# Performance work log

Measured on AMD Instinct MI355X. Metric: run time of the kernel, lower is better.

## Reference

```python
import jax, jax.numpy as jnp
import numpy as np

B, N, E, H = 2, 2048, 1024, 16
D = E // H


def setup_inputs() -> dict:
    key = jax.random.key(0)
    ks = jax.random.split(key, 10)
    s = 0.02  # small init so softmax is well-conditioned
    return {
        "x": jax.random.normal(ks[0], (B, N, E), jnp.float32),
        "y": jax.random.normal(ks[1], (B, N, E), jnp.float32),
        # W stored as [in, out]; torch Linear computes x @ W_t.T + b, equivalent here.
        "Wq": jax.random.normal(ks[2], (E, E), jnp.float32) * s,
        "bq": jax.random.normal(ks[3], (E,), jnp.float32) * s,
        "Wk": jax.random.normal(ks[4], (E, E), jnp.float32) * s,
        "bk": jax.random.normal(ks[5], (E,), jnp.float32) * s,
        "Wv": jax.random.normal(ks[6], (E, E), jnp.float32) * s,
        "bv": jax.random.normal(ks[7], (E,), jnp.float32) * s,
        "Wo": jax.random.normal(ks[8], (E, E), jnp.float32) * s,
        "bo": jax.random.normal(ks[9], (E,), jnp.float32) * s,
    }


def _split_heads(t):
    # [b, n, (h d)] -> [b, h, n, d]
    b, n, e = t.shape
    return t.reshape(b, n, H, D).transpose(0, 2, 1, 3)


def reference(x, y, Wq, bq, Wk, bk, Wv, bv, Wo, bo):
    q = _split_heads(x @ Wq + bq)          # [b,h,n,d]
    k = _split_heads(y @ Wk + bk)
    v = _split_heads(y @ Wv + bv)
    energy = jnp.einsum('bhqd,bhkd->bhqk', q, k)            # [b,h,n,n]
    # Faithful quirk: softmax first, then divide by sqrt(emb_size).
    scaling = jnp.asarray(E, x.dtype) ** 0.5
    att = jax.nn.softmax(energy, axis=-1) / scaling
    out = jnp.einsum('bhqk,bhkd->bhqd', att, v)             # [b,h,n,d]
    out = out.transpose(0, 2, 1, 3).reshape(x.shape[0], x.shape[1], E)
    return out @ Wo + bo
```

## Files before the change

### kernel.cpp

```cpp
#include <hip/hip_runtime.h>
#include <stdint.h>

#define BATCH 2
#define SEQ   2048
#define EMB   1024
#define NH    16
#define HD    64
#define MROWS (BATCH*SEQ)
#define LOG2E 1.4426950408889634f

using bf16x8 = __attribute__((ext_vector_type(8))) short;
using f32x4  = __attribute__((ext_vector_type(4))) float;
using f32x16 = __attribute__((ext_vector_type(16))) float;

__device__ __forceinline__ unsigned short f2bf(float f) {
  __bf16 b = (__bf16)f;
  return __builtin_bit_cast(unsigned short, b);
}

__device__ __forceinline__ unsigned int cvtpk_bf16(float lo, float hi) {
  unsigned int w;
  asm("v_cvt_pk_bf16_f32 %0, %1, %2" : "=v"(w) : "v"(lo), "v"(hi));
  return w;
}

#if __has_builtin(__builtin_amdgcn_exp2f)
__device__ __forceinline__ float fast_exp2(float x) { return __builtin_amdgcn_exp2f(x); }
#else
__device__ __forceinline__ float fast_exp2(float x) {
  float r;
  asm("v_exp_f32 %0, %1\n\ts_nop 1" : "=v"(r) : "v"(x));
  return r;
}
#endif

__device__ __forceinline__ void swap32(unsigned int& a, unsigned int& b, int hi) {
#if __has_builtin(__builtin_amdgcn_permlane32_swap)
  (void)hi;
  typedef unsigned int u32x2_t __attribute__((ext_vector_type(2)));
  u32x2_t r = __builtin_amdgcn_permlane32_swap(a, b, false, false);
  a = r[0]; b = r[1];
#else
  const unsigned int ca = __shfl_xor(a, 32), cb = __shfl_xor(b, 32);
  const unsigned int na = hi ? cb : a;
  const unsigned int nb = hi ? b : ca;
  a = na; b = nb;
#endif
}

__device__ __forceinline__ float xmax32(float x, int hi) {
  unsigned int a = __builtin_bit_cast(unsigned int, x), b = a;
  swap32(a, b, hi);
  return fmaxf(__builtin_bit_cast(float, a), __builtin_bit_cast(float, b));
}

__device__ __forceinline__ float xadd32(float x, int hi) {
  unsigned int a = __builtin_bit_cast(unsigned int, x), b = a;
  swap32(a, b, hi);
  return __builtin_bit_cast(float, a) + __builtin_bit_cast(float, b);
}

__device__ __forceinline__ void async_load16(const void* g, void* l) {
  __builtin_amdgcn_global_load_lds(
      (__attribute__((address_space(1))) void*)g,
      (__attribute__((address_space(3))) void*)l,
      16, 0, 0);
}

__global__ __launch_bounds__(256) void convert_kernel(
    const float* __restrict__ in, unsigned short* __restrict__ out, int n4) {
  int i = blockIdx.x * blockDim.x + threadIdx.x;
  if (i >= n4) return;
  const float4 v = reinterpret_cast<const float4*>(in)[i];
  ushort4 o;
  o.x = f2bf(v.x); o.y = f2bf(v.y); o.z = f2bf(v.z); o.w = f2bf(v.w);
  reinterpret_cast<ushort4*>(out)[i] = o;
}

__global__ __launch_bounds__(256) void transw_kernel(
    const float* __restrict__ Wq, const float* __restrict__ Wk,
    const float* __restrict__ Wv, const float* __restrict__ Wo,
    unsigned short* __restrict__ WtAll) {
  const int z = blockIdx.z;
  const float* W = (z == 0) ? Wq : (z == 1) ? Wk : (z == 2) ? Wv : Wo;
  unsigned short* Wt = WtAll + (size_t)z * EMB * EMB;
  __shared__ unsigned short tile[64][65];
  const int tc = threadIdx.x & 15;
  const int tr = threadIdx.x >> 4;
  const int n0 = blockIdx.x * 64, k0 = blockIdx.y * 64;
#pragma unroll
  for (int rr = 0; rr < 4; ++rr) {
    const int row = rr * 16 + tr;
    float4 v = *reinterpret_cast<const float4*>(W + (size_t)(k0 + row) * EMB + n0 + tc * 4);
    tile[tc * 4 + 0][row] = f2bf(v.x);
    tile[tc * 4 + 1][row] = f2bf(v.y);
    tile[tc * 4 + 2][row] = f2bf(v.z);
    tile[tc * 4 + 3][row] = f2bf(v.w);
  }
  __syncthreads();
#pragma unroll
  for (int rr = 0; rr < 4; ++rr) {
    const int row = rr * 16 + tr;
    ushort4 o;
    o.x = tile[row][tc * 4 + 0];
    o.y = tile[row][tc * 4 + 1];
    o.z = tile[row][tc * 4 + 2];
    o.w = tile[row][tc * 4 + 3];
    *reinterpret_cast<ushort4*>(Wt + (size_t)(n0 + row) * EMB + k0 + tc * 4) = o;
  }
}

#define BM 128
#define BN 128
#define BK 32
#define NKS (EMB/BK)

__global__ __launch_bounds__(256, 3) void gemm_kernel(
    const unsigned short* __restrict__ xb,
    const unsigned short* __restrict__ yb,
    const unsigned short* __restrict__ attnb,
    const unsigned short* __restrict__ WtAll,
    const float* __restrict__ bq, const float* __restrict__ bk,
    const float* __restrict__ bv, const float* __restrict__ bo,
    unsigned short* __restrict__ Qb, unsigned short* __restrict__ Kb,
    unsigned short* __restrict__ Vt, float* __restrict__ dout,
    int phase) {
  __shared__ __align__(16) unsigned short As[3][BM * BK];
  __shared__ __align__(16) unsigned short Bs[3][BN * BK];

  const int z = blockIdx.z;
  const unsigned short* A;
  const unsigned short* Bt;
  const float* bias;
  int mode;
  if (phase == 0) {
    A    = (z == 0) ? xb : yb;
    Bt   = WtAll + (size_t)z * EMB * EMB;
    bias = (z == 0) ? bq : (z == 1) ? bk : bv;
    mode = z;
  } else {
    A = attnb; Bt = WtAll + (size_t)3 * EMB * EMB; bias = bo; mode = 3;
  }

  const int tid = threadIdx.x;
  const int lane = tid & 63, wid = tid >> 6;
  const int wr = wid >> 1, wc = wid & 1;
  const int l15 = lane & 15, l4 = lane >> 4;
  const int m0 = blockIdx.y * BM, n0 = blockIdx.x * BN;

  const int crow = tid >> 2;
  const int cslot = tid & 3;

#define GSTAGE(b, kt)                                                          \
  {                                                                            \
    _Pragma("unroll")                                                          \
    for (int it = 0; it < 2; ++it)                                             \
      async_load16(A + (size_t)(m0 + it * 64 + crow) * EMB + (kt) + cslot * 8, \
                   (char*)As[b] + it * 4096 + wid * 1024);                     \
    _Pragma("unroll")                                                          \
    for (int it = 0; it < 2; ++it)                                             \
      async_load16(Bt + (size_t)(n0 + it * 64 + crow) * EMB + (kt) + cslot * 8,\
                   (char*)Bs[b] + it * 4096 + wid * 1024);                     \
  }

  GSTAGE(0, 0)
  GSTAGE(1, BK)

  f32x4 acc[4][4] = {};

  int buf = 0, sb = 2;
  for (int s = 0; s < NKS; ++s) {
    __builtin_amdgcn_sched_barrier(0);
    if (s < NKS - 1) {
      asm volatile("s_waitcnt vmcnt(4)" ::: "memory");
    } else {
      asm volatile("s_waitcnt vmcnt(0)" ::: "memory");
    }
    __builtin_amdgcn_s_barrier();
    __builtin_amdgcn_sched_barrier(0);

    if (s + 2 < NKS) { GSTAGE(sb, (s + 2) * BK) }

    bf16x8 af[4], bfr[4];
#pragma unroll
    for (int i = 0; i < 4; ++i) {
      af[i]  = *reinterpret_cast<const bf16x8*>((const char*)As[buf] + (wr * 64 + i * 16 + l15) * 64 + l4 * 16);
      bfr[i] = *reinterpret_cast<const bf16x8*>((const char*)Bs[buf] + (wc * 64 + i * 16 + l15) * 64 + l4 * 16);
    }
#pragma unroll
    for (int i = 0; i < 4; ++i)
#pragma unroll
      for (int j = 0; j < 4; ++j)
        acc[i][j] = __builtin_amdgcn_mfma_f32_16x16x32_bf16(af[i], bfr[j], acc[i][j], 0, 0, 0);

    buf = (buf == 2) ? 0 : buf + 1;
    sb  = (sb  == 2) ? 0 : sb + 1;
  }
#undef GSTAGE

#pragma unroll
  for (int i = 0; i < 4; ++i) {
#pragma unroll
    for (int j = 0; j < 4; ++j) {
      const int col = n0 + wc * 64 + j * 16 + l15;
      const float bsv = bias[col];
#pragma unroll
      for (int r = 0; r < 4; ++r) {
        const int row = m0 + wr * 64 + i * 16 + l4 * 4 + r;
        const float v = acc[i][j][r] + bsv;
        if (mode == 3) {
          dout[(size_t)row * EMB + col] = v;
        } else {
          const int b = row >> 11, n = row & (SEQ - 1);
          const int h = col >> 6, d = col & (HD - 1);
          if (mode == 0)
            Qb[(((size_t)(b * NH + h)) * SEQ + n) * HD + d] = f2bf(v);
          else if (mode == 1)
            Kb[(((size_t)(b * NH + h)) * SEQ + n) * HD + d] = f2bf(v * LOG2E);
          else
            Vt[(((size_t)(b * NH + h)) * HD + d) * SEQ + n] = f2bf(v);
        }
      }
    }
  }
}

#define KVB 64
#define NT  (SEQ/KVB)

__global__ __launch_bounds__(256, 2) void flash_kernel(
    const unsigned short* __restrict__ Qb,
    const unsigned short* __restrict__ Kb,
    const unsigned short* __restrict__ Vt,
    unsigned short* __restrict__ attnb) {
  __shared__ __align__(16) char Ks[3][8192];
  __shared__ __align__(16) char Vs[3][8192];

  const int tid = threadIdx.x;
  const int lane = tid & 63, wid = tid >> 6;
  const int l31 = lane & 31, hi = lane >> 5;

  const int lin = blockIdx.x;
  const int swz = (lin & 7) * 64 + (lin >> 3);
  const int bh = swz >> 4;
  const int qt = swz & 15;
  const int bb = bh >> 4, hh = bh & 15;
  const int q0 = qt * 128 + wid * 32;

  const unsigned short* Qp = Qb + (size_t)bh * SEQ * HD;
  const unsigned short* Kp = Kb + (size_t)bh * SEQ * HD;
  const unsigned short* Vp = Vt + (size_t)bh * HD * SEQ;

  const int srow = tid >> 3;
  const int sslot = tid & 7;

  bf16x8 qf[4];
#pragma unroll
  for (int kt = 0; kt < 4; ++kt)
    qf[kt] = *reinterpret_cast<const bf16x8*>(Qp + (size_t)(q0 + l31) * HD + kt * 16 + hi * 8);

#define STAGE(b, kv)                                                        \
  {                                                                         \
    _Pragma("unroll")                                                       \
    for (int it = 0; it < 2; ++it) {                                        \
      const int r = it * 32 + srow;                                         \
      async_load16(Kp + (size_t)((kv) + r) * HD + ((sslot ^ (r & 7)) * 8),  \
                   Ks[b] + it * 4096 + tid * 16);                           \
      async_load16(Vp + (size_t)r * SEQ + (kv) + ((sslot ^ (r & 7)) * 8),   \
                   Vs[b] + it * 4096 + tid * 16);                           \
    }                                                                       \
  }

  STAGE(0, 0)
  STAGE(1, KVB)

  f32x16 accO[2] = {};
  float mI = -1e30f, lI = 0.f;

  int buf = 0, sb = 2;
  for (int t = 0; t < NT; ++t) {
    __builtin_amdgcn_sched_barrier(0);
    if (t < NT - 1) {
      asm volatile("s_waitcnt vmcnt(4)" ::: "memory");
    } else {
      asm volatile("s_waitcnt vmcnt(0)" ::: "memory");
    }
    __builtin_amdgcn_s_barrier();
    __builtin_amdgcn_sched_barrier(0);

    if (t + 2 < NT) { STAGE(sb, (t + 2) * KVB) }

    bf16x8 kf[2][4];
#pragma unroll
    for (int t2 = 0; t2 < 2; ++t2)
#pragma unroll
      for (int kt = 0; kt < 4; ++kt) {
        const int key = t2 * 32 + l31;
        kf[t2][kt] = *reinterpret_cast<const bf16x8*>(
            Ks[buf] + key * 128 + (((kt * 2 + hi) ^ (key & 7)) * 16));
      }
    bf16x8 vf[2][4];
#pragma unroll
    for (int dt = 0; dt < 2; ++dt)
#pragma unroll
      for (int kt = 0; kt < 4; ++kt) {
        const int d = dt * 32 + l31;
        vf[dt][kt] = *reinterpret_cast<const bf16x8*>(
            Vs[buf] + d * 128 + (((kt * 2 + hi) ^ (d & 7)) * 16));
      }

    f32x16 sc[2] = {};
#pragma unroll
    for (int t2 = 0; t2 < 2; ++t2)
#pragma unroll
      for (int kt = 0; kt < 4; ++kt)
        sc[t2] = __builtin_amdgcn_mfma_f32_32x32x16_bf16(kf[t2][kt], qf[kt], sc[t2], 0, 0, 0);

    float mx[8];
#pragma unroll
    for (int i = 0; i < 8; ++i)
      mx[i] = fmaxf(fmaxf(sc[0][i], sc[0][i + 8]), fmaxf(sc[1][i], sc[1][i + 8]));
    mx[0] = fmaxf(mx[0], mx[4]); mx[1] = fmaxf(mx[1], mx[5]);
    mx[2] = fmaxf(mx[2], mx[6]); mx[3] = fmaxf(mx[3], mx[7]);
    float mown = fmaxf(fmaxf(mx[0], mx[1]), fmaxf(mx[2], mx[3]));
    mown = xmax32(mown, hi);

    if (!__all(mown - mI <= 8.0f)) {
      const float mnew = fmaxf(mI, mown);
      const float scl = fast_exp2(mI - mnew);
      mI = mnew;
      lI *= scl;
#pragma unroll
      for (int dt = 0; dt < 2; ++dt)
#pragma unroll
        for (int r = 0; r < 16; ++r) accO[dt][r] *= scl;
    }

    float p[2][16];
    float s4[4] = {0.f, 0.f, 0.f, 0.f};
#pragma unroll
    for (int t2 = 0; t2 < 2; ++t2)
#pragma unroll
      for (int r = 0; r < 16; ++r) {
        p[t2][r] = fast_exp2(sc[t2][r] - mI);
        s4[r & 3] += p[t2][r];
      }
    const float ls = (s4[0] + s4[1]) + (s4[2] + s4[3]);
    lI += xadd32(ls, hi);

    bf16x8 pf[4];
#pragma unroll
    for (int kt = 0; kt < 4; ++kt) {
      const int t2 = kt >> 1, g = (kt & 1) * 8;
      unsigned int Aw = cvtpk_bf16(p[t2][g + 0], p[t2][g + 1]);
      unsigned int Cw = cvtpk_bf16(p[t2][g + 2], p[t2][g + 3]);
      unsigned int Bw = cvtpk_bf16(p[t2][g + 4], p[t2][g + 5]);
      unsigned int Dw = cvtpk_bf16(p[t2][g + 6], p[t2][g + 7]);
      swap32(Aw, Bw, hi);
      swap32(Cw, Dw, hi);
      union { unsigned int u[4]; bf16x8 v; } cvt;
      cvt.u[0] = Aw; cvt.u[1] = Cw; cvt.u[2] = Bw; cvt.u[3] = Dw;
      pf[kt] = cvt.v;
    }

#pragma unroll
    for (int dt = 0; dt < 2; ++dt)
#pragma unroll
      for (int kt = 0; kt < 4; ++kt)
        accO[dt] = __builtin_amdgcn_mfma_f32_32x32x16_bf16(vf[dt][kt], pf[kt], accO[dt], 0, 0, 0);

    buf = (buf == 2) ? 0 : buf + 1;
    sb  = (sb  == 2) ? 0 : sb + 1;
  }
#undef STAGE

  const float inv = 1.0f / (lI * 32.0f);
  const size_t obase = ((size_t)(bb * SEQ + q0 + l31)) * EMB + hh * HD;
#pragma unroll
  for (int dt = 0; dt < 2; ++dt)
#pragma unroll
    for (int rr = 0; rr < 4; ++rr) {
      ushort4 o;
      o.x = f2bf(accO[dt][rr * 4 + 0] * inv);
      o.y = f2bf(accO[dt][rr * 4 + 1] * inv);
      o.z = f2bf(accO[dt][rr * 4 + 2] * inv);
      o.w = f2bf(accO[dt][rr * 4 + 3] * inv);
      *reinterpret_cast<ushort4*>(attnb + obase + dt * 32 + 8 * rr + 4 * hi) = o;
    }
}

extern "C" void kernel_launch(void* const* d_in, const int* in_sizes, int n_in,
                              void* d_out, int out_size, void* d_ws, size_t ws_size,
                              hipStream_t stream) {
  (void)in_sizes; (void)n_in; (void)out_size;
  const float* x  = (const float*)d_in[0];
  const float* y  = (const float*)d_in[1];
  const float* Wq = (const float*)d_in[2];
  const float* bq = (const float*)d_in[3];
  const float* Wk = (const float*)d_in[4];
  const float* bk = (const float*)d_in[5];
  const float* Wv = (const float*)d_in[6];
  const float* bv = (const float*)d_in[7];
  const float* Wo = (const float*)d_in[8];
  const float* bo = (const float*)d_in[9];
  float* out = (float*)d_out;

  char* ws = (char*)d_ws;
  unsigned short* xb    = (unsigned short*)(ws + (size_t)(0u  << 20));
  unsigned short* yb    = (unsigned short*)(ws + (size_t)(8u  << 20));
  unsigned short* WtAll = (unsigned short*)(ws + (size_t)(16u << 20));
  unsigned short* Qb    = (unsigned short*)(ws + (size_t)(24u << 20));
  unsigned short* Kb    = (unsigned short*)(ws + (size_t)(32u << 20));
  unsigned short* Vt    = (unsigned short*)(ws + (size_t)(40u << 20));
  unsigned short* attnb = (unsigned short*)(ws + (size_t)(48u << 20));
  if (ws_size < ((size_t)56u << 20)) return;

  const int n4 = (BATCH * SEQ * EMB) / 4;
  hipLaunchKernelGGL(convert_kernel, dim3(n4 / 256), dim3(256), 0, stream, x, xb, n4);
  hipLaunchKernelGGL(convert_kernel, dim3(n4 / 256), dim3(256), 0, stream, y, yb, n4);
  hipLaunchKernelGGL(transw_kernel, dim3(16, 16, 4), dim3(256), 0, stream, Wq, Wk, Wv, Wo, WtAll);
  hipLaunchKernelGGL(gemm_kernel, dim3(EMB / BN, MROWS / BM, 3), dim3(256), 0, stream,
                     xb, yb, attnb, WtAll, bq, bk, bv, bo, Qb, Kb, Vt, out, 0);
  hipLaunchKernelGGL(flash_kernel, dim3(SEQ / 128 * BATCH * NH), dim3(256), 0, stream,
                     Qb, Kb, Vt, attnb);
  hipLaunchKernelGGL(gemm_kernel, dim3(EMB / BN, MROWS / BM, 1), dim3(256), 0, stream,
                     xb, yb, attnb, WtAll, bq, bk, bv, bo, Qb, Kb, Vt, out, 1);
}
```

Before: 142.6 us.

## Pre-swizzle K/V into MFMA fragment layout and load directly to registers

The QKV GEMM epilogue now writes K and V in a tiled fragment-order layout, so each lane's bf16x8 operand sits contiguously. The flash kernel drops LDS staging and block barriers, runs one 64-thread wave per 32-query block, and software-pipelines K/V global loads straight into registers with double buffering. This removes LDS traffic and synchronisation. The cost is that each wave reloads K/V from global memory/L2 with no sharing across waves, and more registers are used.

```diff
diff --git a/kernel.cpp b/kernel.cpp
--- a/kernel.cpp
+++ b/kernel.cpp
@@ -122,8 +122,8 @@
     const unsigned short* __restrict__ WtAll,
     const float* __restrict__ bq, const float* __restrict__ bk,
     const float* __restrict__ bv, const float* __restrict__ bo,
-    unsigned short* __restrict__ Qb, unsigned short* __restrict__ Kb,
-    unsigned short* __restrict__ Vt, float* __restrict__ dout,
+    unsigned short* __restrict__ Qb, unsigned short* __restrict__ Kf,
+    unsigned short* __restrict__ Vf, float* __restrict__ dout,
     int phase) {
   __shared__ __align__(16) unsigned short As[3][BM * BK];
   __shared__ __align__(16) unsigned short Bs[3][BN * BK];
@@ -213,12 +213,18 @@
         } else {
           const int b = row >> 11, n = row & (SEQ - 1);
           const int h = col >> 6, d = col & (HD - 1);
-          if (mode == 0)
-            Qb[(((size_t)(b * NH + h)) * SEQ + n) * HD + d] = f2bf(v);
-          else if (mode == 1)
-            Kb[(((size_t)(b * NH + h)) * SEQ + n) * HD + d] = f2bf(v * LOG2E);
-          else
-            Vt[(((size_t)(b * NH + h)) * HD + d) * SEQ + n] = f2bf(v);
+          const int bh = b * NH + h;
+          if (mode == 0) {
+            Qb[((size_t)bh * SEQ + n) * HD + d] = f2bf(v);
+          } else if (mode == 1) {
+            const int tile = n >> 6, t2 = (n >> 5) & 1, lk = n & 31;
+            const int g = d >> 3, jj = d & 7;
+            Kf[((size_t)(bh * 32 + tile) * 512 + g * 64 + t2 * 32 + lk) * 8 + jj] = f2bf(v * LOG2E);
+          } else {
+            const int tile = n >> 6, f = (n >> 3) & 7, jj = n & 7;
+            const int dt = d >> 5, lv = d & 31;
+            Vf[((size_t)(bh * 32 + tile) * 512 + f * 64 + dt * 32 + lv) * 8 + jj] = f2bf(v);
+          }
         }
       }
     }
@@ -228,93 +234,59 @@
 #define KVB 64
 #define NT  (SEQ/KVB)
 
-__global__ __launch_bounds__(256, 2) void flash_kernel(
+__global__ __launch_bounds__(64) void flash_kernel(
     const unsigned short* __restrict__ Qb,
-    const unsigned short* __restrict__ Kb,
-    const unsigned short* __restrict__ Vt,
+    const unsigned short* __restrict__ Kf,
+    const unsigned short* __restrict__ Vf,
     unsigned short* __restrict__ attnb) {
-  __shared__ __align__(16) char Ks[3][8192];
-  __shared__ __align__(16) char Vs[3][8192];
-
-  const int tid = threadIdx.x;
-  const int lane = tid & 63, wid = tid >> 6;
+  const int lane = threadIdx.x & 63;
   const int l31 = lane & 31, hi = lane >> 5;
 
   const int lin = blockIdx.x;
-  const int swz = (lin & 7) * 64 + (lin >> 3);
-  const int bh = swz >> 4;
-  const int qt = swz & 15;
+  const int swzid = (lin & 7) * 256 + (lin >> 3);
+  const int bh = swzid >> 6;
+  const int qt = swzid & 63;
   const int bb = bh >> 4, hh = bh & 15;
-  const int q0 = qt * 128 + wid * 32;
+  const int q0 = qt * 32;
 
   const unsigned short* Qp = Qb + (size_t)bh * SEQ * HD;
-  const unsigned short* Kp = Kb + (size_t)bh * SEQ * HD;
-  const unsigned short* Vp = Vt + (size_t)bh * HD * SEQ;
-
-  const int srow = tid >> 3;
-  const int sslot = tid & 7;
+  const bf16x8* K8 = reinterpret_cast<const bf16x8*>(Kf) + (size_t)bh * 32 * 512;
+  const bf16x8* V8 = reinterpret_cast<const bf16x8*>(Vf) + (size_t)bh * 32 * 512;
 
   bf16x8 qf[4];
 #pragma unroll
   for (int kt = 0; kt < 4; ++kt)
     qf[kt] = *reinterpret_cast<const bf16x8*>(Qp + (size_t)(q0 + l31) * HD + kt * 16 + hi * 8);
 
-#define STAGE(b, kv)                                                        \
-  {                                                                         \
-    _Pragma("unroll")                                                       \
-    for (int it = 0; it < 2; ++it) {                                        \
-      const int r = it * 32 + srow;                                         \
-      async_load16(Kp + (size_t)((kv) + r) * HD + ((sslot ^ (r & 7)) * 8),  \
-                   Ks[b] + it * 4096 + tid * 16);                           \
-      async_load16(Vp + (size_t)r * SEQ + (kv) + ((sslot ^ (r & 7)) * 8),   \
-                   Vs[b] + it * 4096 + tid * 16);                           \
-    }                                                                       \
-  }
-
-  STAGE(0, 0)
-  STAGE(1, KVB)
-
   f32x16 accO[2] = {};
   float mI = -1e30f, lI = 0.f;
 
-  int buf = 0, sb = 2;
-  for (int t = 0; t < NT; ++t) {
-    __builtin_amdgcn_sched_barrier(0);
-    if (t < NT - 1) {
-      asm volatile("s_waitcnt vmcnt(4)" ::: "memory");
-    } else {
-      asm volatile("s_waitcnt vmcnt(0)" ::: "memory");
-    }
-    __builtin_amdgcn_s_barrier();
-    __builtin_amdgcn_sched_barrier(0);
-
-    if (t + 2 < NT) { STAGE(sb, (t + 2) * KVB) }
-
-    bf16x8 kf[2][4];
+  bf16x8 kA[2][4], kB[2][4], vb[2][4];
+
+#define LOADK(dst, t)                                                   \
+  {                                                                     \
+    _Pragma("unroll")                                                   \
+    for (int t2 = 0; t2 < 2; ++t2)                                      \
+      _Pragma("unroll")                                                 \
+      for (int kt = 0; kt < 4; ++kt)                                    \
+        dst[t2][kt] = K8[(t) * 512 + (kt * 2 + hi) * 64 + t2 * 32 + l31]; \
+  }
+#define LOADV(t)                                                        \
+  {                                                                     \
+    _Pragma("unroll")                                                   \
+    for (int dt = 0; dt < 2; ++dt)                                      \
+      _Pragma("unroll")                                                 \
+      for (int kt = 0; kt < 4; ++kt)                                    \
+        vb[dt][kt] = V8[(t) * 512 + (kt * 2 + hi) * 64 + dt * 32 + l31]; \
+  }
+
+  auto TILE = [&](bf16x8 (&kc)[2][4]) {
+    f32x16 sc[2] = {};
 #pragma unroll
     for (int t2 = 0; t2 < 2; ++t2)
 #pragma unroll
-      for (int kt = 0; kt < 4; ++kt) {
-        const int key = t2 * 32 + l31;
-        kf[t2][kt] = *reinterpret_cast<const bf16x8*>(
-            Ks[buf] + key * 128 + (((kt * 2 + hi) ^ (key & 7)) * 16));
-      }
-    bf16x8 vf[2][4];
-#pragma unroll
-    for (int dt = 0; dt < 2; ++dt)
-#pragma unroll
-      for (int kt = 0; kt < 4; ++kt) {
-        const int d = dt * 32 + l31;
-        vf[dt][kt] = *reinterpret_cast<const bf16x8*>(
-            Vs[buf] + d * 128 + (((kt * 2 + hi) ^ (d & 7)) * 16));
-      }
-
-    f32x16 sc[2] = {};
-#pragma unroll
-    for (int t2 = 0; t2 < 2; ++t2)
-#pragma unroll
       for (int kt = 0; kt < 4; ++kt)
-        sc[t2] = __builtin_amdgcn_mfma_f32_32x32x16_bf16(kf[t2][kt], qf[kt], sc[t2], 0, 0, 0);
+        sc[t2] = __builtin_amdgcn_mfma_f32_32x32x16_bf16(kc[t2][kt], qf[kt], sc[t2], 0, 0, 0);
 
     float mx[8];
 #pragma unroll
@@ -336,14 +308,13 @@
         for (int r = 0; r < 16; ++r) accO[dt][r] *= scl;
     }
 
-    float p[2][16];
     float s4[4] = {0.f, 0.f, 0.f, 0.f};
 #pragma unroll
     for (int t2 = 0; t2 < 2; ++t2)
 #pragma unroll
       for (int r = 0; r < 16; ++r) {
-        p[t2][r] = fast_exp2(sc[t2][r] - mI);
-        s4[r & 3] += p[t2][r];
+        sc[t2][r] = fast_exp2(sc[t2][r] - mI);
+        s4[r & 3] += sc[t2][r];
       }
     const float ls = (s4[0] + s4[1]) + (s4[2] + s4[3]);
     lI += xadd32(ls, hi);
@@ -352,10 +323,10 @@
 #pragma unroll
     for (int kt = 0; kt < 4; ++kt) {
       const int t2 = kt >> 1, g = (kt & 1) * 8;
-      unsigned int Aw = cvtpk_bf16(p[t2][g + 0], p[t2][g + 1]);
-      unsigned int Cw = cvtpk_bf16(p[t2][g + 2], p[t2][g + 3]);
-      unsigned int Bw = cvtpk_bf16(p[t2][g + 4], p[t2][g + 5]);
-      unsigned int Dw = cvtpk_bf16(p[t2][g + 6], p[t2][g + 7]);
+      unsigned int Aw = cvtpk_bf16(sc[t2][g + 0], sc[t2][g + 1]);
+      unsigned int Cw = cvtpk_bf16(sc[t2][g + 2], sc[t2][g + 3]);
+      unsigned int Bw = cvtpk_bf16(sc[t2][g + 4], sc[t2][g + 5]);
+      unsigned int Dw = cvtpk_bf16(sc[t2][g + 6], sc[t2][g + 7]);
       swap32(Aw, Bw, hi);
       swap32(Cw, Dw, hi);
       union { unsigned int u[4]; bf16x8 v; } cvt;
@@ -367,12 +338,20 @@
     for (int dt = 0; dt < 2; ++dt)
 #pragma unroll
       for (int kt = 0; kt < 4; ++kt)
-        accO[dt] = __builtin_amdgcn_mfma_f32_32x32x16_bf16(vf[dt][kt], pf[kt], accO[dt], 0, 0, 0);
-
-    buf = (buf == 2) ? 0 : buf + 1;
-    sb  = (sb  == 2) ? 0 : sb + 1;
-  }
-#undef STAGE
+        accO[dt] = __builtin_amdgcn_mfma_f32_32x32x16_bf16(vb[dt][kt], pf[kt], accO[dt], 0, 0, 0);
+  };
+
+  LOADK(kA, 0)
+  for (int tt = 0; tt < NT; tt += 2) {
+    LOADV(tt)
+    LOADK(kB, tt + 1)
+    TILE(kA);
+    LOADV(tt + 1)
+    if (tt + 2 < NT) { LOADK(kA, tt + 2) }
+    TILE(kB);
+  }
+#undef LOADK
+#undef LOADV
 
   const float inv = 1.0f / (lI * 32.0f);
   const size_t obase = ((size_t)(bb * SEQ + q0 + l31)) * EMB + hh * HD;
@@ -410,8 +389,8 @@
   unsigned short* yb    = (unsigned short*)(ws + (size_t)(8u  << 20));
   unsigned short* WtAll = (unsigned short*)(ws + (size_t)(16u << 20));
   unsigned short* Qb    = (unsigned short*)(ws + (size_t)(24u << 20));
-  unsigned short* Kb    = (unsigned short*)(ws + (size_t)(32u << 20));
-  unsigned short* Vt    = (unsigned short*)(ws + (size_t)(40u << 20));
+  unsigned short* Kf    = (unsigned short*)(ws + (size_t)(32u << 20));
+  unsigned short* Vf    = (unsigned short*)(ws + (size_t)(40u << 20));
   unsigned short* attnb = (unsigned short*)(ws + (size_t)(48u << 20));
   if (ws_size < ((size_t)56u << 20)) return;
 
@@ -420,9 +399,9 @@
   hipLaunchKernelGGL(convert_kernel, dim3(n4 / 256), dim3(256), 0, stream, y, yb, n4);
   hipLaunchKernelGGL(transw_kernel, dim3(16, 16, 4), dim3(256), 0, stream, Wq, Wk, Wv, Wo, WtAll);
   hipLaunchKernelGGL(gemm_kernel, dim3(EMB / BN, MROWS / BM, 3), dim3(256), 0, stream,
-                     xb, yb, attnb, WtAll, bq, bk, bv, bo, Qb, Kb, Vt, out, 0);
-  hipLaunchKernelGGL(flash_kernel, dim3(SEQ / 128 * BATCH * NH), dim3(256), 0, stream,
-                     Qb, Kb, Vt, attnb);
+                     xb, yb, attnb, WtAll, bq, bk, bv, bo, Qb, Kf, Vf, out, 0);
+  hipLaunchKernelGGL(flash_kernel, dim3(SEQ / 32 * BATCH * NH), dim3(64), 0, stream,
+                     Qb, Kf, Vf, attnb);
   hipLaunchKernelGGL(gemm_kernel, dim3(EMB / BN, MROWS / BM, 1), dim3(256), 0, stream,
-                     xb, yb, attnb, WtAll, bq, bk, bv, bo, Qb, Kb, Vt, out, 1);
-}
+                     xb, yb, attnb, WtAll, bq, bk, bv, bo, Qb, Kf, Vf, out, 1);
+}
```

Result: slower. 151.8 us (+6.4%).
